# Performance work log

Measured on AMD Instinct MI355X. Metric: run time of the kernel, lower is better.

The kernel has to match this reference:

```python
import jax, jax.numpy as jnp
import numpy as np

TEMP = 1.0  # softmax temperature (init kwarg)


def setup_inputs() -> dict:
    key = jax.random.key(0)
    k1, k2 = jax.random.split(key)
    two_n, d_model = 512, 256
    embeddings = jax.random.normal(k1, (two_n, d_model), dtype=jnp.float32)
    targets = jax.random.uniform(k2, (two_n, 1), dtype=jnp.float32)
    return {"embeddings": embeddings, "targets": targets}


def reference(embeddings, targets):
    # embeddings: [2N, d_model], targets: [2N, 1]
    two_n = embeddings.shape[0]
    # label distance d[i,j] = |t_i - t_j|
    d = jnp.abs(targets - targets.T)                                  # [2N, 2N]
    # exp similarity s[i,j] = exp(-||e_i - e_j||_2 / temp)
    diff = embeddings[:, None, :] - embeddings[None, :, :]            # [2N, 2N, d]
    s = jnp.exp(-jnp.linalg.norm(diff, axis=-1) / TEMP)               # [2N, 2N]
    off_diag = 1.0 - jnp.eye(two_n, dtype=s.dtype)                    # [2N, 2N]
    # mask3[i,k,j] = (d[i,j] >= d[i,k]) * (j != i)
    mask3 = (d[:, None, :] >= d[:, :, None]).astype(s.dtype) * off_diag[:, None, :]
    # denominator D[i,k] = sum_j mask3[i,k,j] * s[i,j]
    denom = jnp.einsum('ikj,ij->ik', mask3, s)                        # [2N, 2N]
    loss = jnp.log(s / denom) * off_diag
    return -jnp.sum(loss) / (two_n * (two_n - 1))
```

## Files before the change

kernel.cpp:

```cpp
#include <hip/hip_runtime.h>
#include <math.h>

#define TWO_N 512
#define DM    256
#define NT    256
#define NTR   512

#define OFF_R1    (1u << 20)
#define OFF_TSORT (2u << 20)
#define OFF_INV   ((2u << 20) + 2048)
#define OFF_BSUM  ((2u << 20) + 4096)

#define ACC4(acc, A, B) { float _d;                      \
    _d = (A).x - (B).x; acc += _d * _d;                  \
    _d = (A).y - (B).y; acc += _d * _d;                  \
    _d = (A).z - (B).z; acc += _d * _d;                  \
    _d = (A).w - (B).w; acc += _d * _d; }

__global__ __launch_bounds__(NT) void supcr_dist_rank(
    const float* __restrict__ E, const float* __restrict__ T,
    float* __restrict__ R0, float* __restrict__ R1,
    float* __restrict__ tsort, int* __restrict__ inv)
{
    const int bid = blockIdx.x;
    const int t   = threadIdx.x;

    if (bid > 0) {
        const int tile = bid - 1;
        const int it = (tile >> 1) >> 4, jt = (tile >> 1) & 15, kh = tile & 1;
        __shared__ float4 As4[32 * 33];
        __shared__ float4 Bs4[32 * 33];
        const float4* __restrict__ E4 = reinterpret_cast<const float4*>(E);

        for (int idx = t; idx < 32 * 32; idx += NT) {
            const int row = idx >> 5, c4 = idx & 31;
            As4[row * 33 + c4] = E4[(it * 32 + row) * 64 + kh * 32 + c4];
            Bs4[row * 33 + c4] = E4[(jt * 32 + row) * 64 + kh * 32 + c4];
        }
        __syncthreads();

        const int ty = t >> 4, tx = t & 15;
        float a00 = 0.f, a01 = 0.f, a10 = 0.f, a11 = 0.f;
        #pragma unroll 8
        for (int k4 = 0; k4 < 32; ++k4) {
            const float4 a0 = As4[ty * 33 + k4];
            const float4 a1 = As4[(ty + 16) * 33 + k4];
            const float4 b0 = Bs4[tx * 33 + k4];
            const float4 b1 = Bs4[(tx + 16) * 33 + k4];
            ACC4(a00, a0, b0); ACC4(a01, a0, b1);
            ACC4(a10, a1, b0); ACC4(a11, a1, b1);
        }
        float* __restrict__ Rp = kh ? R1 : R0;
        const int r0 = it * 32 + ty, r1 = r0 + 16;
        const int c0 = jt * 32 + tx, c1 = c0 + 16;
        Rp[r0 * TWO_N + c0] = a00;
        Rp[r0 * TWO_N + c1] = a01;
        Rp[r1 * TWO_N + c0] = a10;
        Rp[r1 * TWO_N + c1] = a11;
    } else {
        __shared__ float Tsh[TWO_N];
        Tsh[t] = T[t]; Tsh[t + 256] = T[t + 256];
        __syncthreads();

        const int ja = t, jb = t + 256;
        const float ta = Tsh[ja], tb = Tsh[jb];
        int rka = 0, rkb = 0;
        const float4* Tsh4 = reinterpret_cast<const float4*>(Tsh);
        #pragma unroll 4
        for (int j4 = 0; j4 < TWO_N / 4; ++j4) {
            const float4 tv = Tsh4[j4];
            const int b0 = 4 * j4, b1 = b0 + 1, b2 = b0 + 2, b3 = b0 + 3;
            rka += (tv.x < ta) || (tv.x == ta && b0 < ja);
            rka += (tv.y < ta) || (tv.y == ta && b1 < ja);
            rka += (tv.z < ta) || (tv.z == ta && b2 < ja);
            rka += (tv.w < ta) || (tv.w == ta && b3 < ja);
            rkb += (tv.x < tb) || (tv.x == tb && b0 < jb);
            rkb += (tv.y < tb) || (tv.y == tb && b1 < jb);
            rkb += (tv.z < tb) || (tv.z == tb && b2 < jb);
            rkb += (tv.w < tb) || (tv.w == tb && b3 < jb);
        }
        tsort[rka] = ta;  inv[ja] = rka;
        tsort[rkb] = tb;  inv[jb] = rkb;
    }
}

__global__ __launch_bounds__(NTR) void supcr_rows(
    const float* __restrict__ T, const float* __restrict__ R0,
    const float* __restrict__ R1, const float* __restrict__ tsort,
    const int* __restrict__ inv, double* __restrict__ bsums)
{
    const int i = blockIdx.x;
    const int k = threadIdx.x;
    const int lane = k & 63, wid = k >> 6;

    __shared__ float  ts[TWO_N];
    __shared__ float  Pe[TWO_N];
    __shared__ double P[TWO_N];
    __shared__ double wsum[8];
    __shared__ double red8[8];

    const float ti  = T[i];
    const float tk  = T[k];
    const float d2  = R0[(size_t)i * TWO_N + k] + R1[(size_t)i * TWO_N + k];
    const float rik = sqrtf(d2);
    const float e   = (k == i) ? 0.f : __expf(-rik);

    ts[k] = tsort[k];
    Pe[inv[k]] = e;
    __syncthreads();

    double v = (double)Pe[k];
    #pragma unroll
    for (int off = 1; off < 64; off <<= 1) {
        const double u = __shfl_up(v, off, 64);
        if (lane >= off) v += u;
    }
    if (lane == 63) wsum[wid] = v;
    __syncthreads();
    double base = 0.0, tot = 0.0;
    #pragma unroll
    for (int w = 0; w < 8; ++w) {
        const double s = wsum[w];
        tot += s;
        if (w < wid) base += s;
    }
    P[k] = v + base;
    const double Stot = tot;
    __syncthreads();

    const int mi = inv[i];

    double local = 0.0;
    if (k != i) {
        const float theta = fabsf(ti - tk);

        const int nl = mi + 1;
        int pos = 0;
        #pragma unroll
        for (int step = 512; step >= 1; step >>= 1) {
            const int np = pos + step;
            if (np <= nl && fabsf(ti - ts[np - 1]) >= theta) pos = np;
        }
        const int cl = nl - pos;

        const int nr = TWO_N - mi;
        int pr = 0;
        #pragma unroll
        for (int step = 512; step >= 1; step >>= 1) {
            const int np = pr + step;
            if (np <= nr && fabsf(ti - ts[mi + np - 1]) < theta) pr = np;
        }
        const int cr = pr;

        double inner = 0.0;
        const int L  = mi - cl + 1;
        const int Rr = mi + cr - 1;
        if (Rr >= L) inner = P[Rr] - ((L > 0) ? P[L - 1] : 0.0);
        const float denom = (float)(Stot - inner);
        local = (double)(-rik - logf(denom));
    }

    #pragma unroll
    for (int off = 32; off > 0; off >>= 1) local += __shfl_down(local, off, 64);
    if (lane == 0) red8[wid] = local;
    __syncthreads();
    if (k == 0) {
        double s = 0.0;
        #pragma unroll
        for (int w = 0; w < 8; ++w) s += red8[w];
        bsums[i] = s;
    }
}

__global__ __launch_bounds__(64) void supcr_finalize(
    const double* __restrict__ bsums, float* __restrict__ out)
{
    const int t = threadIdx.x;
    double s = 0.0;
    #pragma unroll
    for (int w = 0; w < 8; ++w) s += bsums[t + 64 * w];
    #pragma unroll
    for (int off = 32; off > 0; off >>= 1) s += __shfl_down(s, off, 64);
    if (t == 0)
        out[0] = (float)(-s / (double)((long long)TWO_N * (TWO_N - 1)));
}

extern "C" void kernel_launch(void* const* d_in, const int* in_sizes, int n_in,
                              void* d_out, int out_size, void* d_ws, size_t ws_size,
                              hipStream_t stream) {
    (void)in_sizes; (void)n_in; (void)out_size; (void)ws_size;
    const float* E = (const float*)d_in[0];
    const float* T = (const float*)d_in[1];
    float* out = (float*)d_out;

    char* ws = (char*)d_ws;
    float*  R0     = (float*)(ws);
    float*  R1     = (float*)(ws + OFF_R1);
    float*  tsortp = (float*)(ws + OFF_TSORT);
    int*    invp   = (int*)(ws + OFF_INV);
    double* bsums  = (double*)(ws + OFF_BSUM);

    supcr_dist_rank<<<513, NT, 0, stream>>>(E, T, R0, R1, tsortp, invp);
    supcr_rows<<<TWO_N, NTR, 0, stream>>>(T, R0, R1, tsortp, invp, bsums);
    supcr_finalize<<<1, 64, 0, stream>>>(bsums, out);
}
```

Baseline: 93.66 us.

## Use 64x64 distance tiles with 8-way K split and float prefix sums

The distance kernel now computes 64x64 output tiles with a 4x4 register block per thread, splitting the 256-wide feature dimension into 8 slices of 32. Each slice writes its own partial-sum plane, so there are 8 planes instead of 2. The idea is to get more register reuse per shared-memory load while keeping 512 blocks in flight. The rows kernel now sums 8 partial planes instead of 2, which adds global read traffic. Its prefix scan also moves from double to float, making it cheaper but less precise, so the denominator can lose accuracy through cancellation.

```diff
diff --git a/kernel.cpp b/kernel.cpp
--- a/kernel.cpp
+++ b/kernel.cpp
@@ -5,11 +5,12 @@
 #define DM    256
 #define NT    256
 #define NTR   512
-
-#define OFF_R1    (1u << 20)
-#define OFF_TSORT (2u << 20)
-#define OFF_INV   ((2u << 20) + 2048)
-#define OFF_BSUM  ((2u << 20) + 4096)
+#define KS    8
+#define RSTRIDE (TWO_N * TWO_N)
+
+#define OFF_TSORT (8u << 20)
+#define OFF_INV   ((8u << 20) + 2048)
+#define OFF_BSUM  ((8u << 20) + 4096)
 
 #define ACC4(acc, A, B) { float _d;                      \
     _d = (A).x - (B).x; acc += _d * _d;                  \
@@ -19,44 +20,55 @@
 
 __global__ __launch_bounds__(NT) void supcr_dist_rank(
     const float* __restrict__ E, const float* __restrict__ T,
-    float* __restrict__ R0, float* __restrict__ R1,
-    float* __restrict__ tsort, int* __restrict__ inv)
+    float* __restrict__ R, float* __restrict__ tsort, int* __restrict__ inv)
 {
     const int bid = blockIdx.x;
     const int t   = threadIdx.x;
 
-    if (bid > 0) {
-        const int tile = bid - 1;
-        const int it = (tile >> 1) >> 4, jt = (tile >> 1) & 15, kh = tile & 1;
-        __shared__ float4 As4[32 * 33];
-        __shared__ float4 Bs4[32 * 33];
+    if (bid < 512) {
+        __shared__ float4 As4[64 * 9];
+        __shared__ float4 Bs4[64 * 9];
+        const int tile = bid >> 3, ks = bid & 7;
+        const int it = tile >> 3, jt = tile & 7;
         const float4* __restrict__ E4 = reinterpret_cast<const float4*>(E);
 
-        for (int idx = t; idx < 32 * 32; idx += NT) {
-            const int row = idx >> 5, c4 = idx & 31;
-            As4[row * 33 + c4] = E4[(it * 32 + row) * 64 + kh * 32 + c4];
-            Bs4[row * 33 + c4] = E4[(jt * 32 + row) * 64 + kh * 32 + c4];
+        #pragma unroll
+        for (int p = 0; p < 2; ++p) {
+            const int idx = t + p * 256;
+            const int r = idx >> 3, c4 = idx & 7;
+            As4[r * 9 + c4] = E4[(it * 64 + r) * 64 + ks * 8 + c4];
+            Bs4[r * 9 + c4] = E4[(jt * 64 + r) * 64 + ks * 8 + c4];
         }
         __syncthreads();
 
-        const int ty = t >> 4, tx = t & 15;
-        float a00 = 0.f, a01 = 0.f, a10 = 0.f, a11 = 0.f;
-        #pragma unroll 8
-        for (int k4 = 0; k4 < 32; ++k4) {
-            const float4 a0 = As4[ty * 33 + k4];
-            const float4 a1 = As4[(ty + 16) * 33 + k4];
-            const float4 b0 = Bs4[tx * 33 + k4];
-            const float4 b1 = Bs4[(tx + 16) * 33 + k4];
-            ACC4(a00, a0, b0); ACC4(a01, a0, b1);
-            ACC4(a10, a1, b0); ACC4(a11, a1, b1);
-        }
-        float* __restrict__ Rp = kh ? R1 : R0;
-        const int r0 = it * 32 + ty, r1 = r0 + 16;
-        const int c0 = jt * 32 + tx, c1 = c0 + 16;
-        Rp[r0 * TWO_N + c0] = a00;
-        Rp[r0 * TWO_N + c1] = a01;
-        Rp[r1 * TWO_N + c0] = a10;
-        Rp[r1 * TWO_N + c1] = a11;
+        const int tx = t & 15, ty = t >> 4;
+        float acc[4][4];
+        #pragma unroll
+        for (int u = 0; u < 4; ++u)
+            #pragma unroll
+            for (int v = 0; v < 4; ++v) acc[u][v] = 0.f;
+
+        #pragma unroll
+        for (int k4 = 0; k4 < 8; ++k4) {
+            float4 a[4], b[4];
+            #pragma unroll
+            for (int u = 0; u < 4; ++u) a[u] = As4[(ty + 16 * u) * 9 + k4];
+            #pragma unroll
+            for (int v = 0; v < 4; ++v) b[v] = Bs4[(tx + 16 * v) * 9 + k4];
+            #pragma unroll
+            for (int u = 0; u < 4; ++u)
+                #pragma unroll
+                for (int v = 0; v < 4; ++v) ACC4(acc[u][v], a[u], b[v]);
+        }
+
+        float* __restrict__ Rp = R + (size_t)ks * RSTRIDE;
+        #pragma unroll
+        for (int u = 0; u < 4; ++u) {
+            const int row = it * 64 + ty + 16 * u;
+            #pragma unroll
+            for (int v = 0; v < 4; ++v)
+                Rp[row * TWO_N + jt * 64 + tx + 16 * v] = acc[u][v];
+        }
     } else {
         __shared__ float Tsh[TWO_N];
         Tsh[t] = T[t]; Tsh[t + 256] = T[t + 256];
@@ -85,9 +97,9 @@
 }
 
 __global__ __launch_bounds__(NTR) void supcr_rows(
-    const float* __restrict__ T, const float* __restrict__ R0,
-    const float* __restrict__ R1, const float* __restrict__ tsort,
-    const int* __restrict__ inv, double* __restrict__ bsums)
+    const float* __restrict__ T, const float* __restrict__ R,
+    const float* __restrict__ tsort, const int* __restrict__ inv,
+    double* __restrict__ bsums)
 {
     const int i = blockIdx.x;
     const int k = threadIdx.x;
@@ -95,13 +107,17 @@
 
     __shared__ float  ts[TWO_N];
     __shared__ float  Pe[TWO_N];
-    __shared__ double P[TWO_N];
-    __shared__ double wsum[8];
+    __shared__ float  P[TWO_N];
+    __shared__ float  wsumf[8];
     __shared__ double red8[8];
 
-    const float ti  = T[i];
-    const float tk  = T[k];
-    const float d2  = R0[(size_t)i * TWO_N + k] + R1[(size_t)i * TWO_N + k];
+    const float ti = T[i];
+    const float tk = T[k];
+
+    float d2 = 0.f;
+    #pragma unroll
+    for (int p = 0; p < KS; ++p)
+        d2 += R[(size_t)p * RSTRIDE + (size_t)i * TWO_N + k];
     const float rik = sqrtf(d2);
     const float e   = (k == i) ? 0.f : __expf(-rik);
 
@@ -109,23 +125,23 @@
     Pe[inv[k]] = e;
     __syncthreads();
 
-    double v = (double)Pe[k];
+    float v = Pe[k];
     #pragma unroll
     for (int off = 1; off < 64; off <<= 1) {
-        const double u = __shfl_up(v, off, 64);
+        const float u = __shfl_up(v, off, 64);
         if (lane >= off) v += u;
     }
-    if (lane == 63) wsum[wid] = v;
-    __syncthreads();
-    double base = 0.0, tot = 0.0;
+    if (lane == 63) wsumf[wid] = v;
+    __syncthreads();
+    float base = 0.f, tot = 0.f;
     #pragma unroll
     for (int w = 0; w < 8; ++w) {
-        const double s = wsum[w];
+        const float s = wsumf[w];
         tot += s;
         if (w < wid) base += s;
     }
     P[k] = v + base;
-    const double Stot = tot;
+    const float Stot = tot;
     __syncthreads();
 
     const int mi = inv[i];
@@ -152,11 +168,11 @@
         }
         const int cr = pr;
 
-        double inner = 0.0;
+        float inner = 0.f;
         const int L  = mi - cl + 1;
         const int Rr = mi + cr - 1;
-        if (Rr >= L) inner = P[Rr] - ((L > 0) ? P[L - 1] : 0.0);
-        const float denom = (float)(Stot - inner);
+        if (Rr >= L) inner = P[Rr] - ((L > 0) ? P[L - 1] : 0.f);
+        const float denom = Stot - inner;
         local = (double)(-rik - logf(denom));
     }
 
@@ -194,13 +210,12 @@
     float* out = (float*)d_out;
 
     char* ws = (char*)d_ws;
-    float*  R0     = (float*)(ws);
-    float*  R1     = (float*)(ws + OFF_R1);
+    float*  R      = (float*)(ws);
     float*  tsortp = (float*)(ws + OFF_TSORT);
     int*    invp   = (int*)(ws + OFF_INV);
     double* bsums  = (double*)(ws + OFF_BSUM);
 
-    supcr_dist_rank<<<513, NT, 0, stream>>>(E, T, R0, R1, tsortp, invp);
-    supcr_rows<<<TWO_N, NTR, 0, stream>>>(T, R0, R1, tsortp, invp, bsums);
+    supcr_dist_rank<<<513, NT, 0, stream>>>(E, T, R, tsortp, invp);
+    supcr_rows<<<TWO_N, NTR, 0, stream>>>(T, R, tsortp, invp, bsums);
     supcr_finalize<<<1, 64, 0, stream>>>(bsums, out);
 }
```

Result: no change. 93.52 us (-0.2%).
